# Optimization experiments

Measured on AMD Instinct MI355X. Metric: run time of the kernel, lower is better.

The kernel has to match this reference:

```python
import jax, jax.numpy as jnp
import numpy as np

NUM_HEADS = 8
RMS_EPS = 1e-8


def rmsnorm(x, g):
    return x * jax.lax.rsqrt(jnp.mean(x * x, axis=-1, keepdims=True) + RMS_EPS) * g


def activation_quant(x):
    # per-token int8 absmax quant
    scale = 127.0 / jnp.clip(jnp.max(jnp.abs(x), axis=-1, keepdims=True), 1e-5)
    return jnp.clip(jnp.round(x * scale), -128, 127) / scale


def weight_quant(w):
    # ternary (1.58-bit) mean-absmax quant
    scale = 1.0 / jnp.clip(jnp.mean(jnp.abs(w)), 1e-5)
    return jnp.clip(jnp.round(w * scale), -1, 1) / scale


def bitlinear(x, w, g):
    # BitLinear: RMSNorm -> STE-quantized activation @ STE-quantized ternary weight
    xn = rmsnorm(x, g)
    xq = xn + jax.lax.stop_gradient(activation_quant(xn) - xn)
    wq = w + jax.lax.stop_gradient(weight_quant(w) - w)
    return xq @ wq.T


def _attention_pass(q_in, ctx, Wq, gq, Wkv, gkv, A, Bm, mag, Wp, gp):
    B, Nq, C = q_in.shape
    H = NUM_HEADS
    hd = C // H
    scale = hd ** -0.5
    q_proj = bitlinear(q_in, Wq, gq)                       # [B,Nq,C]
    delta = (q_in @ A.T) @ Bm.T                            # DoRA low-rank delta [B,Nq,C]
    q = q_proj.reshape(B, Nq, H, hd).transpose(0, 2, 1, 3)  # [B,H,Nq,hd]
    d = delta.reshape(B, Nq, H, hd).transpose(0, 2, 1, 3)
    q_final = q + mag * d                                  # mag: [1,H,1,1]
    kv = bitlinear(ctx, Wkv, gkv)                          # [B,Nc,2C]
    k, v = jnp.split(kv, 2, axis=-1)
    Nc = ctx.shape[1]
    k = k.reshape(B, Nc, H, hd).transpose(0, 2, 1, 3)
    v = v.reshape(B, Nc, H, hd).transpose(0, 2, 1, 3)
    scores = jnp.einsum('bhqd,bhkd->bhqk', q_final, k) * scale
    out = jnp.einsum('bhqk,bhkd->bhqd', jax.nn.softmax(scores, axis=-1), v)
    out = out.transpose(0, 2, 1, 3).reshape(B, Nq, C)
    return bitlinear(out, Wp, gp)


def setup_inputs() -> dict:
    key = jax.random.key(0)
    ks = jax.random.split(key, 20)
    B, Nx, Nc, D, R = 4, 4096, 1024, 512, 16
    H = NUM_HEADS

    def rn(k, shape, s=0.02):
        return jax.random.normal(k, shape, dtype=jnp.float32) * s

    return {
        'x': jax.random.normal(ks[0], (B, Nx, D), dtype=jnp.float32),
        'c': jax.random.normal(ks[1], (B, Nc, D), dtype=jnp.float32),
        # x-queries-on-c pass
        'W_qx': rn(ks[2], (D, D)), 'g_qx': jnp.ones((D,), jnp.float32),
        'W_kvc': rn(ks[3], (2 * D, D)), 'g_kvc': jnp.ones((D,), jnp.float32),
        'A_x': rn(ks[4], (R, D)), 'B_x': rn(ks[5], (D, R)),
        'mag_x': jnp.ones((1, H, 1, 1), jnp.float32),
        'W_px': rn(ks[6], (D, D)), 'g_px': jnp.ones((D,), jnp.float32),
        # c-queries-on-x pass
        'W_qc': rn(ks[7], (D, D)), 'g_qc': jnp.ones((D,), jnp.float32),
        'W_kvx': rn(ks[8], (2 * D, D)), 'g_kvx': jnp.ones((D,), jnp.float32),
        'A_c': rn(ks[9], (R, D)), 'B_c': rn(ks[10], (D, R)),
        'mag_c': jnp.ones((1, H, 1, 1), jnp.float32),
        'W_pc': rn(ks[11], (D, D)), 'g_pc': jnp.ones((D,), jnp.float32),
    }


def reference(x, c, W_qx, g_qx, W_kvc, g_kvc, A_x, B_x, mag_x, W_px, g_px,
              W_qc, g_qc, W_kvx, g_kvx, A_c, B_c, mag_c, W_pc, g_pc):
    x_out = x + _attention_pass(x, c, W_qx, g_qx, W_kvc, g_kvc, A_x, B_x, mag_x, W_px, g_px)
    c_out = c + _attention_pass(c, x, W_qc, g_qc, W_kvx, g_kvx, A_c, B_c, mag_c, W_pc, g_pc)
    return (x_out, c_out)
```

## Files before the change

### kernel.cpp

```cpp
#include <hip/hip_runtime.h>
#include <math.h>

#define DD 512
#define NHEAD 8
#define HDIM 64

typedef __bf16 bf16x8 __attribute__((ext_vector_type(8)));
typedef unsigned short u16x8 __attribute__((ext_vector_type(8)));
typedef float f32x4 __attribute__((ext_vector_type(4)));

#if __has_builtin(__builtin_amdgcn_exp2f)
#define EXP2F(x) __builtin_amdgcn_exp2f(x)
#else
#define EXP2F(x) exp2f(x)
#endif

#define QSCALE 0.18033688f

static __device__ __forceinline__ unsigned short f2bf(float f) {
    unsigned u = __builtin_bit_cast(unsigned, f);
    u += 0x7fffu + ((u >> 16) & 1u);
    return (unsigned short)(u >> 16);
}
static __device__ __forceinline__ float bf2f(unsigned short u) {
    return __builtin_bit_cast(float, (unsigned)u << 16);
}

static __device__ __forceinline__ float wsum32(const float* __restrict__ part, int mid) {
    int l = threadIdx.x & 63;
    float v = (l < 32) ? part[mid * 32 + l] : 0.f;
#pragma unroll
    for (int o = 16; o > 0; o >>= 1) v += __shfl_xor(v, o);
    return __shfl(v, 0);
}

#define GLOAD16(g, l)                                                          \
    __builtin_amdgcn_global_load_lds(                                          \
        (__attribute__((address_space(1))) void*)(g),                          \
        (__attribute__((address_space(3))) void*)(l), 16, 0, 0)

#define BSTEP(s, hc)                                                           \
    {                                                                          \
        _Pragma("unroll")                                                      \
        for (int i = 0; i < (hc); ++i) {                                       \
            float send = (lane & (s)) ? p[i] : p[i + (hc)];                    \
            float recv = __shfl_xor(send, (s));                                \
            p[i] = ((lane & (s)) ? p[i + (hc)] : p[i]) + recv;                 \
        }                                                                      \
    }

__global__ __launch_bounds__(256) void k_prep1(
    const float* __restrict__ W0, const float* __restrict__ W1,
    const float* __restrict__ W2, const float* __restrict__ W3,
    const float* __restrict__ W4, const float* __restrict__ W5,
    float* __restrict__ part,
    const float* __restrict__ x, const float* __restrict__ c,
    const float* __restrict__ g_qx, const float* __restrict__ g_kvx,
    const float* __restrict__ g_qc, const float* __restrict__ g_kvc,
    unsigned short* __restrict__ a_xq, unsigned short* __restrict__ a_xkv,
    unsigned short* __restrict__ a_cq, unsigned short* __restrict__ a_ckv,
    float* __restrict__ s_xq, float* __restrict__ s_xkv,
    float* __restrict__ s_cq, float* __restrict__ s_ckv,
    const float* __restrict__ A_x, const float* __restrict__ A_c,
    float* __restrict__ tmp_x, float* __restrict__ tmp_c) {
    int t = threadIdx.x;
    if (blockIdx.x < 192) {
        const float* Ws[6] = {W0, W1, W2, W3, W4, W5};
        const int cnt[6] = {262144, 524288, 262144, 262144, 524288, 262144};
        int mid = blockIdx.x >> 5, lb = blockIdx.x & 31;
        const float* W = Ws[mid];
        int n = cnt[mid];
        float s = 0.f;
        for (int i = lb * 256 + t; i < n; i += 32 * 256) s += fabsf(W[i]);
        __shared__ float red[4];
#pragma unroll
        for (int o = 32; o > 0; o >>= 1) s += __shfl_down(s, o);
        if ((t & 63) == 0) red[t >> 6] = s;
        __syncthreads();
        if (t == 0) part[blockIdx.x] = red[0] + red[1] + red[2] + red[3];
        return;
    }
    int w = t >> 6, lane = t & 63;
    int row = (int)(blockIdx.x - 192) * 4 + w;
    bool pc = (row >= 16384);
    int r = pc ? row - 16384 : row;
    const float* xr = (pc ? c : x) + (size_t)r * DD;
    const float* G1 = pc ? g_qc : g_qx;
    const float* G2 = pc ? g_kvc : g_kvx;
    unsigned short* O1 = pc ? a_cq : a_xq;
    unsigned short* O2 = pc ? a_ckv : a_xkv;
    float* S1 = pc ? s_cq : s_xq;
    float* S2 = pc ? s_ckv : s_xkv;
    const float* AM = pc ? A_c : A_x;
    float* TMP = pc ? tmp_c : tmp_x;

    float4 a = *(const float4*)(xr + lane * 8);
    float4 b = *(const float4*)(xr + lane * 8 + 4);
    float p[16];
#pragma unroll
    for (int cc = 0; cc < 16; ++cc) {
        const float4* ar = (const float4*)(AM + (size_t)cc * DD + lane * 8);
        float4 aa = ar[0], ab = ar[1];
        p[cc] = a.x*aa.x + a.y*aa.y + a.z*aa.z + a.w*aa.w
              + b.x*ab.x + b.y*ab.y + b.z*ab.z + b.w*ab.w;
    }
    BSTEP(1, 8) BSTEP(2, 4) BSTEP(4, 2) BSTEP(8, 1)
    p[0] += __shfl_xor(p[0], 16);
    p[0] += __shfl_xor(p[0], 32);
    if (lane < 16) {
        int cidx = ((lane & 1) << 3) | ((lane & 2) << 1) | ((lane & 4) >> 1) | ((lane & 8) >> 3);
        TMP[(size_t)r * 16 + cidx] = p[0];
    }
    float ss = a.x*a.x + a.y*a.y + a.z*a.z + a.w*a.w
             + b.x*b.x + b.y*b.y + b.z*b.z + b.w*b.w;
#pragma unroll
    for (int o = 32; o > 0; o >>= 1) ss += __shfl_xor(ss, o);
    float rn = 1.f / sqrtf(ss * (1.f / 512.f) + 1e-8f);
    const float* gs[2] = {G1, G2};
    unsigned short* os[2] = {O1, O2};
    float* scs[2] = {S1, S2};
#pragma unroll
    for (int pass = 0; pass < 2; ++pass) {
        float4 ga = *(const float4*)(gs[pass] + lane * 8);
        float4 gb = *(const float4*)(gs[pass] + lane * 8 + 4);
        float v[8] = {a.x*rn*ga.x, a.y*rn*ga.y, a.z*rn*ga.z, a.w*rn*ga.w,
                      b.x*rn*gb.x, b.y*rn*gb.y, b.z*rn*gb.z, b.w*rn*gb.w};
        float amax = 0.f;
#pragma unroll
        for (int i = 0; i < 8; ++i) amax = fmaxf(amax, fabsf(v[i]));
#pragma unroll
        for (int o = 32; o > 0; o >>= 1) amax = fmaxf(amax, __shfl_xor(amax, o));
        float mx = fmaxf(amax, 1e-5f);
        float scale = 127.f / mx;
        u16x8 qv;
#pragma unroll
        for (int i = 0; i < 8; ++i) {
            float tq = rintf(v[i] * scale);
            tq = fminf(fmaxf(tq, -128.f), 127.f);
            qv[i] = f2bf(tq);
        }
        *reinterpret_cast<u16x8*>(os[pass] + (size_t)r * DD + lane * 8) = qv;
        if (lane == 0) scs[pass][r] = mx / 127.f;
    }
}

__global__ __launch_bounds__(256) void k_prep2(
    const float* __restrict__ W0, const float* __restrict__ W1,
    const float* __restrict__ W2, const float* __restrict__ W3,
    const float* __restrict__ W4, const float* __restrict__ W5,
    const float* __restrict__ part, unsigned short* __restrict__ Wq,
    const float* __restrict__ tmp_x, const float* __restrict__ tmp_c,
    const float* __restrict__ B_x, const float* __restrict__ B_c,
    unsigned short* __restrict__ qf1, unsigned short* __restrict__ qf2) {
    if (blockIdx.x < 8192) {
        int e = blockIdx.x * 256 + threadIdx.x;
        const float* Ws[6] = {W0, W1, W2, W3, W4, W5};
        int mid, base;
        if (e < 262144)       { mid = 0; base = 0; }
        else if (e < 786432)  { mid = 1; base = 262144; }
        else if (e < 1048576) { mid = 2; base = 786432; }
        else if (e < 1310720) { mid = 3; base = 1048576; }
        else if (e < 1835008) { mid = 4; base = 1310720; }
        else                  { mid = 5; base = 1835008; }
        float cnt = (mid == 1 || mid == 4) ? 524288.f : 262144.f;
        float mean = fmaxf(wsum32(part, mid) / cnt, 1e-5f);
        float sc = 1.f / mean;
        float t = rintf(Ws[mid][e - base] * sc);
        t = fminf(fmaxf(t, -1.f), 1.f);
        Wq[e] = f2bf(t);
        return;
    }
    int idx = (int)(blockIdx.x - 8192) * 256 + threadIdx.x;
    int m2 = idx >> 9, n2 = idx & 511;
    const float* tr;
    const float* br;
    unsigned short* out;
    if (m2 < 16384) {
        tr = tmp_x + (size_t)m2 * 16; br = B_x + (size_t)n2 * 16; out = qf1 + idx;
    } else {
        tr = tmp_c + (size_t)(m2 - 16384) * 16; br = B_c + (size_t)n2 * 16;
        out = qf2 + (idx - 8388608);
    }
    const float4* t4 = (const float4*)tr;
    const float4* b4 = (const float4*)br;
    float acc = 0.f;
#pragma unroll
    for (int rr = 0; rr < 4; ++rr) {
        float4 ta = t4[rr], ba = b4[rr];
        acc += ta.x*ba.x + ta.y*ba.y + ta.z*ba.z + ta.w*ba.w;
    }
    *out = f2bf(acc);
}

__global__ __launch_bounds__(256) void k_rmsq_combine(
    const unsigned short* __restrict__ Op_a, const float* __restrict__ Lp_a,
    const float* __restrict__ g_a, unsigned short* __restrict__ out_a,
    float* __restrict__ sc_a,
    const unsigned short* __restrict__ Op_b, const float* __restrict__ Lp_b,
    const float* __restrict__ g_b, unsigned short* __restrict__ out_b,
    float* __restrict__ sc_b) {
    int w = threadIdx.x >> 6, lane = threadIdx.x & 63;
    int row = (int)blockIdx.x * 4 + w;
    bool pb = (row >= 16384);
    int r = pb ? row - 16384 : row;
    int S = pb ? 4 : 1;
    int lognq = pb ? 10 : 12;
    const unsigned short* Op = pb ? Op_b : Op_a;
    const float* Lp = pb ? Lp_b : Lp_a;
    const float* g  = pb ? g_b : g_a;
    unsigned short* out = pb ? out_b : out_a;
    float* a_inv = pb ? sc_b : sc_a;

    int Nq = 1 << lognq;
    int b = r >> lognq, q = r & (Nq - 1);
    int h = lane >> 3;
    float l = 0.f;
    float u[8] = {};
    for (int s = 0; s < S; ++s) {
        l += Lp[((size_t)(s * 4 + b) * 8 + h) * Nq + q];
        u16x8 ov = *reinterpret_cast<const u16x8*>(
            Op + ((size_t)(s * 4 + b) * Nq + q) * 512 + lane * 8);
#pragma unroll
        for (int i = 0; i < 8; ++i) u[i] += bf2f(ov[i]);
    }
    float invl = 1.f / l;
#pragma unroll
    for (int i = 0; i < 8; ++i) u[i] *= invl;
    float ss = 0.f;
#pragma unroll
    for (int i = 0; i < 8; ++i) ss += u[i] * u[i];
#pragma unroll
    for (int o = 32; o > 0; o >>= 1) ss += __shfl_xor(ss, o);
    float rn = 1.f / sqrtf(ss * (1.f / 512.f) + 1e-8f);
    float4 ga = *(const float4*)(g + lane * 8);
    float4 gb = *(const float4*)(g + lane * 8 + 4);
    float v[8] = {u[0]*rn*ga.x, u[1]*rn*ga.y, u[2]*rn*ga.z, u[3]*rn*ga.w,
                  u[4]*rn*gb.x, u[5]*rn*gb.y, u[6]*rn*gb.z, u[7]*rn*gb.w};
    float amax = 0.f;
#pragma unroll
    for (int i = 0; i < 8; ++i) amax = fmaxf(amax, fabsf(v[i]));
#pragma unroll
    for (int o = 32; o > 0; o >>= 1) amax = fmaxf(amax, __shfl_xor(amax, o));
    float mx = fmaxf(amax, 1e-5f);
    float scale = 127.f / mx;
    u16x8 qv;
#pragma unroll
    for (int i = 0; i < 8; ++i) {
        float tq = rintf(v[i] * scale);
        tq = fminf(fmaxf(tq, -128.f), 127.f);
        qv[i] = f2bf(tq);
    }
    *reinterpret_cast<u16x8*>(out + (size_t)r * DD + lane * 8) = qv;
    if (lane == 0) a_inv[r] = mx / 127.f;
}

__global__ __launch_bounds__(256) void k_gemm_qkv(
    const unsigned short* __restrict__ a3_a, const unsigned short* __restrict__ a3_b,
    const unsigned short* __restrict__ w3_a, const unsigned short* __restrict__ w3_b,
    const float* __restrict__ ai3_a, const float* __restrict__ ai3_b,
    const float* __restrict__ mag_a, const float* __restrict__ mag_b,
    const unsigned short* __restrict__ dl_a, const unsigned short* __restrict__ dl_b,
    unsigned short* __restrict__ Qb_a, unsigned short* __restrict__ Qb_b,
    const unsigned short* __restrict__ a4_a, const unsigned short* __restrict__ a4_b,
    const unsigned short* __restrict__ w4_a, const unsigned short* __restrict__ w4_b,
    const float* __restrict__ ai4_a, const float* __restrict__ ai4_b,
    unsigned short* __restrict__ Kb_a, unsigned short* __restrict__ Kb_b,
    unsigned short* __restrict__ Vt_a, unsigned short* __restrict__ Vt_b,
    const float* __restrict__ part) {
    __shared__ __align__(16) unsigned short sA[128 * 32];
    __shared__ __align__(16) unsigned short sB[128 * 32];
    int bid = blockIdx.x;
    bool isQ = (bid >= 1280);
    const unsigned short *Aq, *Wq;
    const float* a_inv;
    int m0, n0, logn, mid;
    float cnt;
    bool pb;
    if (!isQ) {
        int g = bid & 7, k = bid >> 3;
        n0 = (k & 7) * 128;
        int my = (k >> 3) * 8 + g;
        pb = my >= 32;
        m0 = (pb ? my - 32 : my) * 128;
        Aq = pb ? a4_b : a4_a;  Wq = pb ? w4_b : w4_a;
        a_inv = pb ? ai4_b : ai4_a;
        logn = pb ? 12 : 10;
        mid = pb ? 4 : 1; cnt = 524288.f;
    } else {
        int b2 = bid - 1280;
        int g = b2 & 7, k = b2 >> 3;
        n0 = (k & 3) * 128;
        int my = (k >> 2) * 8 + g;
        pb = my >= 128;
        m0 = (pb ? my - 128 : my) * 128;
        Aq = pb ? a3_b : a3_a;  Wq = pb ? w3_b : w3_a;
        a_inv = pb ? ai3_b : ai3_a;
        logn = pb ? 10 : 12;
        mid = pb ? 3 : 0; cnt = 262144.f;
    }
    float wv = fmaxf(wsum32(part, mid) / cnt, 1e-5f);

    int t = threadIdx.x;
    int w = t >> 6, lane = t & 63;
    int wm = w >> 1, wn = w & 1;
    int lr = lane & 15, lg = lane >> 4;
    int row_st = t >> 2, chunk = t & 3;
    f32x4 acc[4][4] = {};

    for (int k0 = 0; k0 < 512; k0 += 32) {
        __syncthreads();
#pragma unroll
        for (int i = 0; i < 2; ++i) {
            int row = i * 64 + row_st;
            GLOAD16(Aq + (size_t)(m0 + row) * 512 + k0 + chunk * 8, sA + ((size_t)i * 256 + t) * 8);
            GLOAD16(Wq + (size_t)(n0 + row) * 512 + k0 + chunk * 8, sB + ((size_t)i * 256 + t) * 8);
        }
        asm volatile("s_waitcnt vmcnt(0)" ::: "memory");
        __syncthreads();
        bf16x8 af[4], bfr[4];
#pragma unroll
        for (int mt = 0; mt < 4; ++mt)
            af[mt] = *reinterpret_cast<const bf16x8*>(&sA[(wm * 64 + mt * 16 + lr) * 32 + lg * 8]);
#pragma unroll
        for (int nt = 0; nt < 4; ++nt)
            bfr[nt] = *reinterpret_cast<const bf16x8*>(&sB[(wn * 64 + nt * 16 + lr) * 32 + lg * 8]);
#pragma unroll
        for (int mt = 0; mt < 4; ++mt)
#pragma unroll
            for (int nt = 0; nt < 4; ++nt)
                acc[mt][nt] = __builtin_amdgcn_mfma_f32_16x16x32_bf16(af[mt], bfr[nt], acc[mt][nt], 0, 0, 0);
    }

    if (!isQ) {
        unsigned short* OutB = pb ? Kb_b : Kb_a;
        unsigned short* OutB2 = pb ? Vt_b : Vt_a;
        const bool isV = (n0 >= 512);
        const int Nc = 1 << logn;
#pragma unroll
        for (int mt = 0; mt < 4; ++mt) {
            int mb = m0 + wm * 64 + mt * 16 + lg * 4;
            int b = mb >> logn, key = mb & (Nc - 1);
            float as_[4];
#pragma unroll
            for (int r = 0; r < 4; ++r) as_[r] = a_inv[mb + r] * wv;
#pragma unroll
            for (int nt = 0; nt < 4; ++nt) {
                int n = n0 + wn * 64 + nt * 16 + lr;
                int n2 = isV ? (n - 512) : n;
                int h = n2 >> 6, dd = n2 & 63;
                if (isV) {
                    int i0 = key & 31;
                    int keyp = (key & ~31) | (((i0 >> 2) & 3) * 8 + ((i0 >> 4) & 1) * 4);
                    ushort4 v;
                    v.x = f2bf(acc[mt][nt][0] * as_[0]);
                    v.y = f2bf(acc[mt][nt][1] * as_[1]);
                    v.z = f2bf(acc[mt][nt][2] * as_[2]);
                    v.w = f2bf(acc[mt][nt][3] * as_[3]);
                    *reinterpret_cast<ushort4*>(
                        OutB2 + ((size_t)(b * NHEAD + h) * 64 + dd) * Nc + keyp) = v;
                } else {
#pragma unroll
                    for (int r = 0; r < 4; ++r)
                        OutB[((size_t)(b * NHEAD + h) * Nc + key + r) * 64 + dd] =
                            f2bf(acc[mt][nt][r] * as_[r]);
                }
            }
        }
    } else {
        const float* Extra = pb ? mag_b : mag_a;
        const unsigned short* Dlt = pb ? dl_b : dl_a;
        unsigned short* OutB = pb ? Qb_b : Qb_a;
#pragma unroll
        for (int mt = 0; mt < 4; ++mt) {
#pragma unroll
            for (int r = 0; r < 4; ++r) {
                int m = m0 + wm * 64 + mt * 16 + lg * 4 + r;
                float as = a_inv[m] * wv;
                int b = m >> logn, q = m & ((1 << logn) - 1);
#pragma unroll
                for (int nt = 0; nt < 4; ++nt) {
                    int n = n0 + wn * 64 + nt * 16 + lr;
                    float dl = bf2f(Dlt[(size_t)m * 512 + n]);
                    float val = acc[mt][nt][r] * as + Extra[n >> 6] * dl;
                    int h = n >> 6, d = n & 63;
                    OutB[((((size_t)(b * NHEAD + h)) << logn) + q) * 64 + d] =
                        f2bf(val * QSCALE);
                }
            }
        }
    }
}

__global__ __launch_bounds__(256) void k_gemm_out(
    const unsigned short* __restrict__ a_a, const unsigned short* __restrict__ a_b,
    const unsigned short* __restrict__ w_a, const unsigned short* __restrict__ w_b,
    const float* __restrict__ ai_a, const float* __restrict__ ai_b,
    const float* __restrict__ part,
    const float* __restrict__ Ex_a, const float* __restrict__ Ex_b,
    float* __restrict__ OF_a, float* __restrict__ OF_b) {
    __shared__ __align__(16) unsigned short sA[128 * 32];
    __shared__ __align__(16) unsigned short sB[128 * 32];
    int bid = blockIdx.x;
    int g = bid & 7, k = bid >> 3;
    int n0 = (k & 3) * 128;
    int my = (k >> 2) * 8 + g;
    bool pb = (my >= 128);
    int m0 = (pb ? my - 128 : my) * 128;
    const unsigned short* Aq = pb ? a_b : a_a;
    const unsigned short* Wq = pb ? w_b : w_a;
    const float* a_inv = pb ? ai_b : ai_a;
    const float* Extra = pb ? Ex_b : Ex_a;
    float* OutF = pb ? OF_b : OF_a;
    float wv = fmaxf(wsum32(part, pb ? 5 : 2) / 262144.f, 1e-5f);

    int t = threadIdx.x;
    int w = t >> 6, lane = t & 63;
    int wm = w >> 1, wn = w & 1;
    int lr = lane & 15, lg = lane >> 4;
    int row_st = t >> 2, chunk = t & 3;
    f32x4 acc[4][4] = {};

    for (int k0 = 0; k0 < 512; k0 += 32) {
        __syncthreads();
#pragma unroll
        for (int i = 0; i < 2; ++i) {
            int row = i * 64 + row_st;
            GLOAD16(Aq + (size_t)(m0 + row) * 512 + k0 + chunk * 8, sA + ((size_t)i * 256 + t) * 8);
            GLOAD16(Wq + (size_t)(n0 + row) * 512 + k0 + chunk * 8, sB + ((size_t)i * 256 + t) * 8);
        }
        asm volatile("s_waitcnt vmcnt(0)" ::: "memory");
        __syncthreads();
        bf16x8 af[4], bfr[4];
#pragma unroll
        for (int mt = 0; mt < 4; ++mt)
            af[mt] = *reinterpret_cast<const bf16x8*>(&sA[(wm * 64 + mt * 16 + lr) * 32 + lg * 8]);
#pragma unroll
        for (int nt = 0; nt < 4; ++nt)
            bfr[nt] = *reinterpret_cast<const bf16x8*>(&sB[(wn * 64 + nt * 16 + lr) * 32 + lg * 8]);
#pragma unroll
        for (int mt = 0; mt < 4; ++mt)
#pragma unroll
            for (int nt = 0; nt < 4; ++nt)
                acc[mt][nt] = __builtin_amdgcn_mfma_f32_16x16x32_bf16(af[mt], bfr[nt], acc[mt][nt], 0, 0, 0);
    }

#pragma unroll
    for (int mt = 0; mt < 4; ++mt) {
#pragma unroll
        for (int r = 0; r < 4; ++r) {
            int m = m0 + wm * 64 + mt * 16 + lg * 4 + r;
            float as = a_inv[m] * wv;
#pragma unroll
            for (int nt = 0; nt < 4; ++nt) {
                int n = n0 + wn * 64 + nt * 16 + lr;
                size_t idx = (size_t)m * 512 + n;
                OutF[idx] = acc[mt][nt][r] * as + Extra[idx];
            }
        }
    }
}

__global__ __launch_bounds__(512) void k_attn_mfma(
    const unsigned short* __restrict__ Qb_a, const unsigned short* __restrict__ Kb_a,
    const unsigned short* __restrict__ Vt_a, unsigned short* __restrict__ Op_a,
    float* __restrict__ Lp_a,
    const unsigned short* __restrict__ Qb_b, const unsigned short* __restrict__ Kb_b,
    const unsigned short* __restrict__ Vt_b, unsigned short* __restrict__ Op_b,
    float* __restrict__ Lp_b) {
    __shared__ unsigned short sK[2][64][72];
    __shared__ unsigned short sVt[2][64][72];
    int t = threadIdx.x;
    int w = t >> 6, lane = t & 63;
    int lr = lane & 15, lg = lane >> 4;

    int bid = blockIdx.x;
    bool pb = (bid < 512);
    int lb = pb ? bid : bid - 512;
    const unsigned short* Qb = pb ? Qb_b : Qb_a;
    const unsigned short* Kb = pb ? Kb_b : Kb_a;
    const unsigned short* Vt = pb ? Vt_b : Vt_a;
    unsigned short* Opart = pb ? Op_b : Op_a;
    float* Lpart = pb ? Lp_b : Lp_a;
    int Nq = pb ? 1024 : 4096;
    int Nc = pb ? 4096 : 1024;
    int S = pb ? 4 : 1;
    int LOGS = pb ? 2 : 0;
    int nqs = pb ? 2 : 4;

    int j = lb >> 3;
    int s = j & (S - 1);
    int j2 = j >> LOGS;
    int qblk = j2 & ((1 << nqs) - 1);
    int bh = ((lb & 7) << 2) | (j2 >> nqs);
    int b = bh >> 3, h = bh & 7;
    int q0 = qblk * 256 + w * 32;

    bf16x8 aq[2][2];
#pragma unroll
    for (int qt = 0; qt < 2; ++qt) {
        const unsigned short* qbase = Qb + ((size_t)bh * Nq + q0 + qt * 16 + lr) * 64 + lg * 8;
        aq[qt][0] = *reinterpret_cast<const bf16x8*>(qbase);
        aq[qt][1] = *reinterpret_cast<const bf16x8*>(qbase + 32);
    }

    u16x8 ou;
#pragma unroll
    for (int jj = 0; jj < 8; ++jj) ou[jj] = (lr == 0) ? 0x3F80 : 0;
    bf16x8 onesf = __builtin_bit_cast(bf16x8, ou);

    f32x4 o[2][4] = {};
    f32x4 osum[2] = {};

    const unsigned short* kglob = Kb + (size_t)bh * Nc * 64;
    const unsigned short* vglob = Vt + (size_t)bh * 64 * (size_t)Nc;

    int srow = t >> 3, sseg = t & 7;
    const unsigned short* kptr = kglob + (size_t)srow * 64 + sseg * 8;
    const unsigned short* vptr = vglob + (size_t)srow * Nc + sseg * 8;

    int kts = s * (Nc >> LOGS);
    int nt = (Nc >> LOGS) >> 6;

    bf16x8 rK = *reinterpret_cast<const bf16x8*>(kptr + (size_t)kts * 64);
    bf16x8 rV = *reinterpret_cast<const bf16x8*>(vptr + kts);
    *reinterpret_cast<bf16x8*>(&sK[0][srow][sseg * 8]) = rK;
    *reinterpret_cast<bf16x8*>(&sVt[0][srow][sseg * 8]) = rV;
    rK = *reinterpret_cast<const bf16x8*>(kptr + (size_t)(kts + 64) * 64);
    rV = *reinterpret_cast<const bf16x8*>(vptr + kts + 64);
    __syncthreads();

    int cur = 0;
    for (int ti = 0; ti < nt; ++ti) {
        if (ti + 1 < nt) {
            *reinterpret_cast<bf16x8*>(&sK[cur ^ 1][srow][sseg * 8]) = rK;
            *reinterpret_cast<bf16x8*>(&sVt[cur ^ 1][srow][sseg * 8]) = rV;
            if (ti + 2 < nt) {
                int knext = kts + (ti + 2) * 64;
                rK = *reinterpret_cast<const bf16x8*>(kptr + (size_t)knext * 64);
                rV = *reinterpret_cast<const bf16x8*>(vptr + knext);
            }
        }
#pragma unroll
        for (int half = 0; half < 2; ++half) {
            bf16x8 pa0, pa1;
#pragma unroll
            for (int ki = 0; ki < 2; ++ki) {
                int kt = half * 2 + ki;
                bf16x8 bk0 = *reinterpret_cast<const bf16x8*>(&sK[cur][kt * 16 + lr][lg * 8]);
                bf16x8 bk1 = *reinterpret_cast<const bf16x8*>(&sK[cur][kt * 16 + lr][32 + lg * 8]);
                f32x4 a0 = {}, a1 = {};
                __builtin_amdgcn_s_setprio(1);
                a0 = __builtin_amdgcn_mfma_f32_16x16x32_bf16(bk0, aq[0][0], a0, 0, 0, 0);
                a1 = __builtin_amdgcn_mfma_f32_16x16x32_bf16(bk0, aq[1][0], a1, 0, 0, 0);
                a0 = __builtin_amdgcn_mfma_f32_16x16x32_bf16(bk1, aq[0][1], a0, 0, 0, 0);
                a1 = __builtin_amdgcn_mfma_f32_16x16x32_bf16(bk1, aq[1][1], a1, 0, 0, 0);
                __builtin_amdgcn_s_setprio(0);
                const int hb = ki * 4;
#pragma unroll
                for (int r = 0; r < 4; ++r) {
                    pa0[hb + r] = (__bf16)EXP2F(a0[r]);
                    pa1[hb + r] = (__bf16)EXP2F(a1[r]);
                }
            }
            __builtin_amdgcn_s_setprio(1);
#pragma unroll
            for (int dt = 0; dt < 4; ++dt) {
                bf16x8 vb = *reinterpret_cast<const bf16x8*>(&sVt[cur][dt * 16 + lr][half * 32 + lg * 8]);
                o[0][dt] = __builtin_amdgcn_mfma_f32_16x16x32_bf16(pa0, vb, o[0][dt], 0, 0, 0);
                o[1][dt] = __builtin_amdgcn_mfma_f32_16x16x32_bf16(pa1, vb, o[1][dt], 0, 0, 0);
            }
            osum[0] = __builtin_amdgcn_mfma_f32_16x16x32_bf16(pa0, onesf, osum[0], 0, 0, 0);
            osum[1] = __builtin_amdgcn_mfma_f32_16x16x32_bf16(pa1, onesf, osum[1], 0, 0, 0);
            __builtin_amdgcn_s_setprio(0);
        }
        __syncthreads();
        cur ^= 1;
    }
    unsigned short* obase = Opart + ((size_t)(s * 4 + b) * Nq + q0) * 512 + h * 64;
#pragma unroll
    for (int qt = 0; qt < 2; ++qt)
#pragma unroll
        for (int dt = 0; dt < 4; ++dt)
#pragma unroll
            for (int r = 0; r < 4; ++r)
                obase[(size_t)(qt * 16 + lg * 4 + r) * 512 + dt * 16 + lr] = f2bf(o[qt][dt][r]);
    if (lr == 0) {
        float* lbase = Lpart + ((size_t)(s * 4 + b) * 8 + h) * Nq + q0;
#pragma unroll
        for (int qt = 0; qt < 2; ++qt)
#pragma unroll
            for (int r = 0; r < 4; ++r)
                lbase[qt * 16 + lg * 4 + r] = osum[qt][r];
    }
}

extern "C" void kernel_launch(void* const* d_in, const int* in_sizes, int n_in,
                              void* d_out, int out_size, void* d_ws, size_t ws_size,
                              hipStream_t stream) {
    const float* x     = (const float*)d_in[0];
    const float* c     = (const float*)d_in[1];
    const float* Wq_x  = (const float*)d_in[2];
    const float* g_qx  = (const float*)d_in[3];
    const float* Wkv_c = (const float*)d_in[4];
    const float* g_kvc = (const float*)d_in[5];
    const float* A_x   = (const float*)d_in[6];
    const float* B_x   = (const float*)d_in[7];
    const float* mag_x = (const float*)d_in[8];
    const float* Wp_x  = (const float*)d_in[9];
    const float* g_px  = (const float*)d_in[10];
    const float* Wq_c  = (const float*)d_in[11];
    const float* g_qc  = (const float*)d_in[12];
    const float* Wkv_x = (const float*)d_in[13];
    const float* g_kvx = (const float*)d_in[14];
    const float* A_c   = (const float*)d_in[15];
    const float* B_c   = (const float*)d_in[16];
    const float* mag_c = (const float*)d_in[17];
    const float* Wp_c  = (const float*)d_in[18];
    const float* g_pc  = (const float*)d_in[19];

    float* ws = (float*)d_ws;
    unsigned short* Wb = (unsigned short*)ws;
    const size_t Woff[6] = {0, 262144, 786432, 1048576, 1310720, 1835008};
    float* part  = ws + 1048576;
    float* sc_xq  = ws + 1049600;
    float* sc_xkv = sc_xq + 16384;
    float* sc_cq  = sc_xkv + 16384;
    float* sc_ckv = sc_cq + 4096;
    float* sc_o1  = sc_ckv + 4096;
    float* sc_o2  = sc_o1 + 16384;
    float* tmp_x  = ws + 1111040;
    float* tmp_c  = tmp_x + 262144;
    float* actblk = ws + 1438720;
    unsigned short* act_xq  = (unsigned short*)actblk;
    unsigned short* act_xkv = (unsigned short*)(actblk + 4194304);
    unsigned short* act_cq  = (unsigned short*)(actblk + 8388608);
    unsigned short* act_ckv = (unsigned short*)(actblk + 9437184);
    unsigned short* Opart1 = (unsigned short*)actblk;
    float* qf1_f  = ws + 11924480;
    unsigned short* Opart2 = (unsigned short*)qf1_f;
    float* qf2_f  = ws + 16118784;
    float* Qb1_f  = ws + 17167360;
    float* Qb2_f  = ws + 21361664;
    float* Kb1_f  = ws + 22410240;
    float* Vt1_f  = ws + 23458816;
    float* Kb2_f  = ws + 24507392;
    float* Vt2_f  = ws + 28701696;
    float* Lpart1 = ws + 32896000;
    float* Lpart2 = ws + 33027072;

    unsigned short* qf1 = (unsigned short*)qf1_f;
    unsigned short* qf2 = (unsigned short*)qf2_f;
    unsigned short* Qb1 = (unsigned short*)Qb1_f;
    unsigned short* Qb2 = (unsigned short*)Qb2_f;
    unsigned short* Kb1 = (unsigned short*)Kb1_f;
    unsigned short* Vt1 = (unsigned short*)Vt1_f;
    unsigned short* Kb2 = (unsigned short*)Kb2_f;
    unsigned short* Vt2 = (unsigned short*)Vt2_f;
    unsigned short* act_o1 = Qb1;
    unsigned short* act_o2 = Qb2;

    size_t need = (size_t)33158144 * sizeof(float);
    if (ws_size < need) return;

    float* outx = (float*)d_out;
    float* outc = outx + (size_t)4 * 4096 * 512;

    k_prep1<<<5312, 256, 0, stream>>>(Wq_x, Wkv_c, Wp_x, Wq_c, Wkv_x, Wp_c, part,
                                      x, c, g_qx, g_kvx, g_qc, g_kvc,
                                      act_xq, act_xkv, act_cq, act_ckv,
                                      sc_xq, sc_xkv, sc_cq, sc_ckv,
                                      A_x, A_c, tmp_x, tmp_c);
    k_prep2<<<49152, 256, 0, stream>>>(Wq_x, Wkv_c, Wp_x, Wq_c, Wkv_x, Wp_c, part, Wb,
                                       tmp_x, tmp_c, B_x, B_c, qf1, qf2);
    k_gemm_qkv<<<1920, 256, 0, stream>>>(
        act_xq, act_cq, Wb + Woff[0], Wb + Woff[3], sc_xq, sc_cq,
        mag_x, mag_c, qf1, qf2, Qb1, Qb2,
        act_ckv, act_xkv, Wb + Woff[1], Wb + Woff[4], sc_ckv, sc_xkv,
        Kb1, Kb2, Vt1, Vt2, part);
    k_attn_mfma<<<1024, 512, 0, stream>>>(Qb1, Kb1, Vt1, Opart1, Lpart1,
                                          Qb2, Kb2, Vt2, Opart2, Lpart2);
    k_rmsq_combine<<<5120, 256, 0, stream>>>(Opart1, Lpart1, g_px, act_o1, sc_o1,
                                             Opart2, Lpart2, g_pc, act_o2, sc_o2);
    k_gemm_out<<<640, 256, 0, stream>>>(
        act_o1, act_o2, Wb + Woff[2], Wb + Woff[5], sc_o1, sc_o2, part,
        x, c, outx, outc);
}
```

Before: 272.4 us.

## Double-buffer LDS tiles in QKV and output GEMM K-loops

Replaces the single-buffered K-loop in both projection GEMM kernels with a ping-pong LDS scheme. The next K-slice is fetched with global_load_lds while MFMAs run on the current one, and MFMA issue priority is raised with s_setprio. The goal is to hide global-load latency behind compute and drop one barrier per iteration. In exchange, LDS use per block doubles to 32 KB, which may reduce occupancy.

```diff
diff --git a/kernel.cpp b/kernel.cpp
--- a/kernel.cpp
+++ b/kernel.cpp
@@ -46,6 +46,53 @@
             float send = (lane & (s)) ? p[i] : p[i + (hc)];                    \
             float recv = __shfl_xor(send, (s));                                \
             p[i] = ((lane & (s)) ? p[i + (hc)] : p[i]) + recv;                 \
+        }                                                                      \
+    }
+
+#define GEMM_KLOOP(Aq, Wq, m0, n0)                                             \
+    {                                                                          \
+        _Pragma("unroll")                                                      \
+        for (int i = 0; i < 2; ++i) {                                          \
+            int row = i * 64 + row_st;                                         \
+            GLOAD16(Aq + (size_t)((m0) + row) * 512 + chunk * 8,               \
+                    sA[0] + ((size_t)i * 256 + t) * 8);                        \
+            GLOAD16(Wq + (size_t)((n0) + row) * 512 + chunk * 8,               \
+                    sB[0] + ((size_t)i * 256 + t) * 8);                        \
+        }                                                                      \
+        asm volatile("s_waitcnt vmcnt(0)" ::: "memory");                       \
+        __syncthreads();                                                       \
+        int cur = 0;                                                           \
+        for (int k0 = 0; k0 < 512; k0 += 32) {                                 \
+            if (k0 + 32 < 512) {                                               \
+                _Pragma("unroll")                                              \
+                for (int i = 0; i < 2; ++i) {                                  \
+                    int row = i * 64 + row_st;                                 \
+                    GLOAD16(Aq + (size_t)((m0) + row) * 512 + k0 + 32 + chunk * 8, \
+                            sA[cur ^ 1] + ((size_t)i * 256 + t) * 8);          \
+                    GLOAD16(Wq + (size_t)((n0) + row) * 512 + k0 + 32 + chunk * 8, \
+                            sB[cur ^ 1] + ((size_t)i * 256 + t) * 8);          \
+                }                                                              \
+            }                                                                  \
+            bf16x8 af[4], bfr[4];                                              \
+            _Pragma("unroll")                                                  \
+            for (int mt = 0; mt < 4; ++mt)                                     \
+                af[mt] = *reinterpret_cast<const bf16x8*>(                     \
+                    &sA[cur][(wm * 64 + mt * 16 + lr) * 32 + lg * 8]);         \
+            _Pragma("unroll")                                                  \
+            for (int nt = 0; nt < 4; ++nt)                                     \
+                bfr[nt] = *reinterpret_cast<const bf16x8*>(                    \
+                    &sB[cur][(wn * 64 + nt * 16 + lr) * 32 + lg * 8]);         \
+            __builtin_amdgcn_s_setprio(1);                                     \
+            _Pragma("unroll")                                                  \
+            for (int mt = 0; mt < 4; ++mt)                                     \
+                _Pragma("unroll")                                              \
+                for (int nt = 0; nt < 4; ++nt)                                 \
+                    acc[mt][nt] = __builtin_amdgcn_mfma_f32_16x16x32_bf16(     \
+                        af[mt], bfr[nt], acc[mt][nt], 0, 0, 0);                \
+            __builtin_amdgcn_s_setprio(0);                                     \
+            asm volatile("s_waitcnt vmcnt(0)" ::: "memory");                   \
+            __syncthreads();                                                   \
+            cur ^= 1;                                                          \
         }                                                                      \
     }
 
@@ -267,8 +314,8 @@
     unsigned short* __restrict__ Kb_a, unsigned short* __restrict__ Kb_b,
     unsigned short* __restrict__ Vt_a, unsigned short* __restrict__ Vt_b,
     const float* __restrict__ part) {
-    __shared__ __align__(16) unsigned short sA[128 * 32];
-    __shared__ __align__(16) unsigned short sB[128 * 32];
+    __shared__ __align__(16) unsigned short sA[2][128 * 32];
+    __shared__ __align__(16) unsigned short sB[2][128 * 32];
     int bid = blockIdx.x;
     bool isQ = (bid >= 1280);
     const unsigned short *Aq, *Wq;
@@ -307,29 +354,7 @@
     int row_st = t >> 2, chunk = t & 3;
     f32x4 acc[4][4] = {};
 
-    for (int k0 = 0; k0 < 512; k0 += 32) {
-        __syncthreads();
-#pragma unroll
-        for (int i = 0; i < 2; ++i) {
-            int row = i * 64 + row_st;
-            GLOAD16(Aq + (size_t)(m0 + row) * 512 + k0 + chunk * 8, sA + ((size_t)i * 256 + t) * 8);
-            GLOAD16(Wq + (size_t)(n0 + row) * 512 + k0 + chunk * 8, sB + ((size_t)i * 256 + t) * 8);
-        }
-        asm volatile("s_waitcnt vmcnt(0)" ::: "memory");
-        __syncthreads();
-        bf16x8 af[4], bfr[4];
-#pragma unroll
-        for (int mt = 0; mt < 4; ++mt)
-            af[mt] = *reinterpret_cast<const bf16x8*>(&sA[(wm * 64 + mt * 16 + lr) * 32 + lg * 8]);
-#pragma unroll
-        for (int nt = 0; nt < 4; ++nt)
-            bfr[nt] = *reinterpret_cast<const bf16x8*>(&sB[(wn * 64 + nt * 16 + lr) * 32 + lg * 8]);
-#pragma unroll
-        for (int mt = 0; mt < 4; ++mt)
-#pragma unroll
-            for (int nt = 0; nt < 4; ++nt)
-                acc[mt][nt] = __builtin_amdgcn_mfma_f32_16x16x32_bf16(af[mt], bfr[nt], acc[mt][nt], 0, 0, 0);
-    }
+    GEMM_KLOOP(Aq, Wq, m0, n0)
 
     if (!isQ) {
         unsigned short* OutB = pb ? Kb_b : Kb_a;
@@ -398,8 +423,8 @@
     const float* __restrict__ part,
     const float* __restrict__ Ex_a, const float* __restrict__ Ex_b,
     float* __restrict__ OF_a, float* __restrict__ OF_b) {
-    __shared__ __align__(16) unsigned short sA[128 * 32];
-    __shared__ __align__(16) unsigned short sB[128 * 32];
+    __shared__ __align__(16) unsigned short sA[2][128 * 32];
+    __shared__ __align__(16) unsigned short sB[2][128 * 32];
     int bid = blockIdx.x;
     int g = bid & 7, k = bid >> 3;
     int n0 = (k & 3) * 128;
@@ -420,29 +445,7 @@
     int row_st = t >> 2, chunk = t & 3;
     f32x4 acc[4][4] = {};
 
-    for (int k0 = 0; k0 < 512; k0 += 32) {
-        __syncthreads();
-#pragma unroll
-        for (int i = 0; i < 2; ++i) {
-            int row = i * 64 + row_st;
-            GLOAD16(Aq + (size_t)(m0 + row) * 512 + k0 + chunk * 8, sA + ((size_t)i * 256 + t) * 8);
-            GLOAD16(Wq + (size_t)(n0 + row) * 512 + k0 + chunk * 8, sB + ((size_t)i * 256 + t) * 8);
-        }
-        asm volatile("s_waitcnt vmcnt(0)" ::: "memory");
-        __syncthreads();
-        bf16x8 af[4], bfr[4];
-#pragma unroll
-        for (int mt = 0; mt < 4; ++mt)
-            af[mt] = *reinterpret_cast<const bf16x8*>(&sA[(wm * 64 + mt * 16 + lr) * 32 + lg * 8]);
-#pragma unroll
-        for (int nt = 0; nt < 4; ++nt)
-            bfr[nt] = *reinterpret_cast<const bf16x8*>(&sB[(wn * 64 + nt * 16 + lr) * 32 + lg * 8]);
-#pragma unroll
-        for (int mt = 0; mt < 4; ++mt)
-#pragma unroll
-            for (int nt = 0; nt < 4; ++nt)
-                acc[mt][nt] = __builtin_amdgcn_mfma_f32_16x16x32_bf16(af[mt], bfr[nt], acc[mt][nt], 0, 0, 0);
-    }
+    GEMM_KLOOP(Aq, Wq, m0, n0)
 
 #pragma unroll
     for (int mt = 0; mt < 4; ++mt) {
```

Result: no change. 271.4 us (-0.4%).
